# Performance work log

Measured on AMD Instinct MI355X. Metric: run time of the kernel, lower is better.

The kernel has to match this reference:

```python
import jax, jax.numpy as jnp
import numpy as np

VOCAB, EMB, HID, FC1, NCLS = 32000, 2048, 2048, 256, 3
T, B = 256, 128


def setup_inputs() -> dict:
    key = jax.random.key(0)
    ks = jax.random.split(key, 10)
    s_e = 1.0  # torch Embedding default init N(0,1)
    s_h = 1.0 / np.sqrt(HID)
    s_f1 = 1.0 / np.sqrt(HID)
    s_f2 = 1.0 / np.sqrt(FC1)
    return {
        "x": jax.random.randint(ks[0], (T, B), 0, VOCAB, dtype=jnp.int64)
        if jax.config.jax_enable_x64 else jax.random.randint(ks[0], (T, B), 0, VOCAB, dtype=jnp.int32),
        "emb": jax.random.normal(ks[1], (VOCAB, EMB), dtype=jnp.float32) * s_e,
        "W_ih": jax.random.uniform(ks[2], (HID, EMB), jnp.float32, -s_h, s_h),
        "W_hh": jax.random.uniform(ks[3], (HID, HID), jnp.float32, -s_h, s_h),
        "b_ih": jax.random.uniform(ks[4], (HID,), jnp.float32, -s_h, s_h),
        "b_hh": jax.random.uniform(ks[5], (HID,), jnp.float32, -s_h, s_h),
        "fc1_w": jax.random.uniform(ks[6], (FC1, HID), jnp.float32, -s_f1, s_f1),
        "fc1_b": jax.random.uniform(ks[7], (FC1,), jnp.float32, -s_f1, s_f1),
        "fc2_w": jax.random.uniform(ks[8], (NCLS, FC1), jnp.float32, -s_f2, s_f2),
        "fc2_b": jax.random.uniform(ks[9], (NCLS,), jnp.float32, -s_f2, s_f2),
    }


def reference(x, emb, W_ih, W_hh, b_ih, b_hh, fc1_w, fc1_b, fc2_w, fc2_b):
    # Embedding: [T, B] -> [T, B, E]
    xe = emb[x]
    # Precompute input projections for all steps in one big GEMM: [T, B, H]
    xproj = jnp.einsum("tbe,he->tbh", xe, W_ih) + b_ih + b_hh
    h0 = jnp.zeros((x.shape[1], W_hh.shape[0]), dtype=xe.dtype)

    def step(h, xp_t):
        h = jnp.tanh(xp_t + h @ W_hh.T)
        return h, None

    h_last, _ = jax.lax.scan(step, h0, xproj)
    # MLP head: hidden -> 256 -> relu -> 3
    z = jax.nn.relu(h_last @ fc1_w.T + fc1_b)
    return z @ fc2_w.T + fc2_b
```

## Files before the change

### kernel.cpp

```cpp
#include <hip/hip_runtime.h>

typedef _Float16 half8 __attribute__((ext_vector_type(8)));
typedef _Float16 half4v __attribute__((ext_vector_type(4)));
typedef float float4v __attribute__((ext_vector_type(4)));

#define HID 2048
#define EMBD 2048
#define BATCH 128
#define TSTEPS 256
#define STEP ((size_t)BATCH * HID)

__global__ __launch_bounds__(256) void cast_f16_kernel(const float* __restrict__ src,
                                                       _Float16* __restrict__ dst, int n) {
    int i = (blockIdx.x * 256 + threadIdx.x) * 4;
    int stride = gridDim.x * 256 * 4;
    for (; i < n; i += stride) {
        float4v v = *(const float4v*)(src + i);
        half4v h;
        h[0] = (_Float16)v[0]; h[1] = (_Float16)v[1];
        h[2] = (_Float16)v[2]; h[3] = (_Float16)v[3];
        *(half4v*)(dst + i) = h;
    }
}

__global__ __launch_bounds__(256) void bias_kernel(const float* __restrict__ a,
                                                   const float* __restrict__ b,
                                                   float* __restrict__ dst) {
    int i = blockIdx.x * 256 + threadIdx.x;
    if (i < HID) dst[i] = a[i] + b[i];
}

__global__ __launch_bounds__(256) void phaseA_kernel(const int* __restrict__ x,
                                                     const float* __restrict__ emb,
                                                     const _Float16* __restrict__ w16,
                                                     const float* __restrict__ bias,
                                                     _Float16* __restrict__ xproj) {
    __shared__ __align__(16) _Float16 As[128 * 64];
    __shared__ __align__(16) _Float16 Bs[128 * 64];

    const int tid = threadIdx.x;
    const int bx  = blockIdx.x;
    const int nt = bx & 15, mt = bx >> 4;
    const long m0 = (long)mt * 128;
    const long n0 = (long)nt * 128;
    const int lane = tid & 63, w = tid >> 6;
    const int ln15 = lane & 15, kg = lane >> 4;
    const int wr = (w >> 1) * 64, wc = (w & 1) * 64;

    int xr[4];
#pragma unroll
    for (int it = 0; it < 4; ++it) xr[it] = x[m0 + ((it * 256 + tid) >> 3)];

    float4v acc[4][4];
#pragma unroll
    for (int m = 0; m < 4; ++m)
#pragma unroll
        for (int n = 0; n < 4; ++n) acc[m][n] = (float4v){0.f, 0.f, 0.f, 0.f};

    for (int kt = 0; kt < 32; ++kt) {
        __syncthreads();
#pragma unroll
        for (int it = 0; it < 4; ++it) {
            int c = it * 256 + tid;
            const float* src = emb + (long)xr[it] * EMBD + kt * 64 + (c & 7) * 8;
            float4v v0 = *(const float4v*)src;
            float4v v1 = *(const float4v*)(src + 4);
            half8 hv;
#pragma unroll
            for (int q = 0; q < 4; ++q) { hv[q] = (_Float16)v0[q]; hv[4 + q] = (_Float16)v1[q]; }
            *(half8*)(&As[c * 8]) = hv;
        }
#pragma unroll
        for (int it = 0; it < 4; ++it) {
            int c = it * 256 + tid;
            const _Float16* src = w16 + (n0 + (c >> 3)) * (long)EMBD + kt * 64 + (c & 7) * 8;
            __builtin_amdgcn_global_load_lds((const __attribute__((address_space(1))) void*)src,
                                             (__attribute__((address_space(3))) void*)&Bs[c * 8],
                                             16, 0, 0);
        }
        __syncthreads();
#pragma unroll
        for (int kk = 0; kk < 2; ++kk) {
            half8 a[4], b[4];
#pragma unroll
            for (int m = 0; m < 4; ++m)
                a[m] = *(half8*)(&As[(wr + m * 16 + ln15) * 64 + kk * 32 + kg * 8]);
#pragma unroll
            for (int n = 0; n < 4; ++n)
                b[n] = *(half8*)(&Bs[(wc + n * 16 + ln15) * 64 + kk * 32 + kg * 8]);
#pragma unroll
            for (int m = 0; m < 4; ++m)
#pragma unroll
                for (int n = 0; n < 4; ++n)
                    acc[m][n] = __builtin_amdgcn_mfma_f32_16x16x32_f16(b[n], a[m], acc[m][n], 0, 0, 0);
        }
    }
#pragma unroll
    for (int m = 0; m < 4; ++m) {
        long mg = m0 + wr + m * 16 + ln15;
#pragma unroll
        for (int n = 0; n < 4; ++n) {
            int nb = (int)n0 + wc + n * 16 + kg * 4;
            float4v bv = *(const float4v*)(bias + nb);
            union { half4v h; unsigned long long u; } pk;
#pragma unroll
            for (int r = 0; r < 4; ++r) pk.h[r] = (_Float16)(acc[m][n][r] + bv[r]);
            *(unsigned long long*)(xproj + mg * HID + nb) = pk.u;
        }
    }
}

__global__ __launch_bounds__(256, 1) void scan_kernel(_Float16* __restrict__ xb,
                                                      const _Float16* __restrict__ whh,
                                                      float* __restrict__ hlast,
                                                      unsigned char* __restrict__ flags) {
    __shared__ __align__(16) _Float16 Wl[32 * 2048];
    __shared__ float part[4][16 * 33];

    const int tid = threadIdx.x;
    const int bx = blockIdx.x;
    const int gid = bx & 3, sub = bx >> 2;
    const int m0 = gid * 32, n0 = sub * 32;
    const int lane = tid & 63, w = tid >> 6;
    const int ln15 = lane & 15, kg = lane >> 4;
    const int pr = w >> 1, kh = w & 1;

    for (int it = 0; it < 32; ++it) {
        int c = it * 256 + tid;
        int col = c >> 8, ch = c & 255;
        half8 v = *(const half8*)(whh + (long)(n0 + col) * HID + ch * 8);
        *(half8*)((char*)Wl + col * 4096 + ((ch * 16) ^ ((col & 7) << 4))) = v;
    }
    __syncthreads();

    unsigned char* gfl = flags + gid * 64;
    const unsigned long long* gfl64 = (const unsigned long long*)gfl;
    const size_t arow = (size_t)(m0 + pr * 16 + ln15);
    const int wb0 = ln15 * 4096, wb1 = (16 + ln15) * 4096;
    const int swz = (ln15 & 7) << 4;
    const int kb = kh * 2048;
    const int rp = tid >> 7, ridx = tid & 127;
    const int rrow = ridx >> 3, rc4 = (ridx & 7) * 4;
    const size_t oidx = (size_t)(m0 + rp * 16 + rrow) * HID + n0 + rc4;

    for (int s = 0; s < TSTEPS; ++s) {
        unsigned long long xbits = __hip_atomic_load(
            (const unsigned long long*)(xb + (size_t)(s + 1) * STEP + oidx),
            __ATOMIC_RELAXED, __HIP_MEMORY_SCOPE_AGENT);

        float4v acc0 = (float4v){0.f, 0.f, 0.f, 0.f};
        float4v acc1 = (float4v){0.f, 0.f, 0.f, 0.f};
        if (s > 0) {
            unsigned long long pat =
                (unsigned long long)(unsigned char)(s - 1) * 0x0101010101010101ull;
            for (;;) {
                bool ok = true;
                if (lane < 8) {
                    unsigned long long v = __hip_atomic_load(gfl64 + lane,
                                            __ATOMIC_RELAXED, __HIP_MEMORY_SCOPE_AGENT);
                    unsigned long long xx = v ^ pat;
                    ok = !((xx - 0x0101010101010101ull) & ~xx & 0x8080808080808080ull);
                }
                if (__all(ok)) break;
            }
            asm volatile("" ::: "memory");
            __builtin_amdgcn_sched_barrier(0);

            const _Float16* hrow = xb + (size_t)(s - 1) * STEP + arow * HID + kh * 1024;
#pragma unroll
            for (int j = 0; j < 32; ++j) {
                half8 a = *(const half8*)(hrow + j * 32 + kg * 8);
                int k2 = kb + j * 64 + kg * 16;
                half8 b0 = *(half8*)((char*)Wl + wb0 + (k2 ^ swz));
                half8 b1 = *(half8*)((char*)Wl + wb1 + (k2 ^ swz));
                acc0 = __builtin_amdgcn_mfma_f32_16x16x32_f16(a, b0, acc0, 0, 0, 0);
                acc1 = __builtin_amdgcn_mfma_f32_16x16x32_f16(a, b1, acc1, 0, 0, 0);
            }
#pragma unroll
            for (int r = 0; r < 4; ++r) {
                part[w][(kg * 4 + r) * 33 + ln15] = acc0[r];
                part[w][(kg * 4 + r) * 33 + 16 + ln15] = acc1[r];
            }
        }

        float s0 = 0.f, s1 = 0.f, s2 = 0.f, s3 = 0.f;
        if (s > 0) {
            __syncthreads();
            const float* p0 = &part[2 * rp][rrow * 33 + rc4];
            const float* p1 = &part[2 * rp + 1][rrow * 33 + rc4];
            s0 = p0[0] + p1[0]; s1 = p0[1] + p1[1];
            s2 = p0[2] + p1[2]; s3 = p0[3] + p1[3];
        }
        union { unsigned long long u; half4v h; } xbv; xbv.u = xbits;
        float o0 = tanhf(s0 + (float)xbv.h[0]);
        float o1 = tanhf(s1 + (float)xbv.h[1]);
        float o2 = tanhf(s2 + (float)xbv.h[2]);
        float o3 = tanhf(s3 + (float)xbv.h[3]);

        if (s < TSTEPS - 1) {
            union { half4v h; unsigned long long u; } pk;
            pk.h[0] = (_Float16)o0; pk.h[1] = (_Float16)o1;
            pk.h[2] = (_Float16)o2; pk.h[3] = (_Float16)o3;
            __hip_atomic_store((unsigned long long*)(xb + (size_t)s * STEP + oidx),
                               pk.u, __ATOMIC_RELAXED, __HIP_MEMORY_SCOPE_AGENT);
            __syncthreads();
            if (tid == 0)
                __hip_atomic_store(&gfl[sub], (unsigned char)(s + 1),
                                   __ATOMIC_RELAXED, __HIP_MEMORY_SCOPE_AGENT);
        } else {
            float4v f = {o0, o1, o2, o3};
            *(float4v*)(hlast + oidx) = f;
        }
    }
}

__global__ __launch_bounds__(256) void fc1_kernel(const float* __restrict__ hlast,
                                                  const float* __restrict__ w,
                                                  const float* __restrict__ b,
                                                  float* __restrict__ z) {
    __shared__ float hs[8][256];
    const int blk = blockIdx.x;
    const int j = threadIdx.x;
    const int bb0 = blk * 8;
    float acc[8];
#pragma unroll
    for (int r = 0; r < 8; ++r) acc[r] = 0.f;
    const float* wr = w + (long)j * HID;
    const int sr = j >> 5, sc = (j & 31) * 8;

    for (int kt = 0; kt < 8; ++kt) {
        __syncthreads();
        float4v h0 = *(const float4v*)(hlast + (long)(bb0 + sr) * HID + kt * 256 + sc);
        float4v h1 = *(const float4v*)(hlast + (long)(bb0 + sr) * HID + kt * 256 + sc + 4);
        *(float4v*)&hs[sr][sc] = h0;
        *(float4v*)&hs[sr][sc + 4] = h1;
        __syncthreads();
        for (int k = 0; k < 256; k += 4) {
            float4v wv = *(const float4v*)(wr + kt * 256 + k);
#pragma unroll
            for (int r = 0; r < 8; ++r) {
                float4v hv = *(const float4v*)&hs[r][k];
                acc[r] += hv[0] * wv[0] + hv[1] * wv[1] + hv[2] * wv[2] + hv[3] * wv[3];
            }
        }
    }
    float bj = b[j];
#pragma unroll
    for (int r = 0; r < 8; ++r) z[(bb0 + r) * 256 + j] = fmaxf(acc[r] + bj, 0.f);
}

__global__ __launch_bounds__(256) void fc2_kernel(const float* __restrict__ z,
                                                  const float* __restrict__ w,
                                                  const float* __restrict__ b,
                                                  float* __restrict__ out) {
    __shared__ float red[4];
    int bb = blockIdx.x;
    int tid = threadIdx.x;
    float zv = z[bb * 256 + tid];
    for (int c = 0; c < 3; ++c) {
        float s = zv * w[c * 256 + tid];
        for (int off = 32; off > 0; off >>= 1) s += __shfl_down(s, off, 64);
        if ((tid & 63) == 0) red[tid >> 6] = s;
        __syncthreads();
        if (tid == 0) out[bb * 3 + c] = red[0] + red[1] + red[2] + red[3] + b[c];
        __syncthreads();
    }
}

extern "C" void kernel_launch(void* const* d_in, const int* in_sizes, int n_in,
                              void* d_out, int out_size, void* d_ws, size_t ws_size,
                              hipStream_t stream) {
    const int*   x    = (const int*)d_in[0];
    const float* emb  = (const float*)d_in[1];
    const float* Wih  = (const float*)d_in[2];
    const float* Whh  = (const float*)d_in[3];
    const float* bih  = (const float*)d_in[4];
    const float* bhh  = (const float*)d_in[5];
    const float* fc1w = (const float*)d_in[6];
    const float* fc1b = (const float*)d_in[7];
    const float* fc2w = (const float*)d_in[8];
    const float* fc2b = (const float*)d_in[9];
    float* out = (float*)d_out;

    char* ws = (char*)d_ws;
    size_t off = 0;
    _Float16* xb    = (_Float16*)(ws + off); off += 257 * STEP * 2;
    _Float16* wih16 = (_Float16*)(ws + off); off += (size_t)HID * EMBD * 2;
    _Float16* whh16 = (_Float16*)(ws + off); off += (size_t)HID * HID * 2;
    float*    bias  = (float*)(ws + off);    off += (size_t)HID * 4;
    float*    hlast = (float*)(ws + off);    off += (size_t)BATCH * HID * 4;
    float*    z     = (float*)(ws + off);    off += (size_t)BATCH * 256 * 4;
    unsigned char* flags = (unsigned char*)(ws + off); off += 256;

    hipMemsetAsync(flags, 0, 256, stream);

    cast_f16_kernel<<<4096, 256, 0, stream>>>(Wih, wih16, HID * EMBD);
    cast_f16_kernel<<<4096, 256, 0, stream>>>(Whh, whh16, HID * HID);
    bias_kernel<<<8, 256, 0, stream>>>(bih, bhh, bias);

    phaseA_kernel<<<4096, 256, 0, stream>>>(x, emb, wih16, bias, xb + STEP);

    void* args[] = {(void*)&xb, (void*)&whh16, (void*)&hlast, (void*)&flags};
    hipLaunchCooperativeKernel((const void*)scan_kernel, dim3(256), dim3(256), args, 0, stream);

    fc1_kernel<<<16, 256, 0, stream>>>(hlast, fc1w, fc1b, z);
    fc2_kernel<<<BATCH, 256, 0, stream>>>(z, fc2w, fc2b, out);
}
```

Baseline: 2.731 ms.

## Map scan blocks to XCDs with K-split pairs exchanging partial sums

Each scan block reads its hardware XCC id and takes a slot from a per-XCD atomic counter. Blocks are assigned so each XCD handles one batch group and one K half, with 64 output columns per block. Paired blocks on the two K halves exchange partial sums through a global buffer, and per-XCD flag arrays use monotonic counters plus s_sleep. The aim is to keep the h-state polling and traffic local to an XCD's L2 and to cut cross-XCD synchronization. The cost is an extra cross-block partial-sum handoff each step, and correctness relies on an even block distribution across XCDs. Phase A also replaces global_load_lds with a plain load and store.

```diff
diff --git a/kernel.cpp b/kernel.cpp
--- a/kernel.cpp
+++ b/kernel.cpp
@@ -74,9 +74,7 @@
         for (int it = 0; it < 4; ++it) {
             int c = it * 256 + tid;
             const _Float16* src = w16 + (n0 + (c >> 3)) * (long)EMBD + kt * 64 + (c & 7) * 8;
-            __builtin_amdgcn_global_load_lds((const __attribute__((address_space(1))) void*)src,
-                                             (__attribute__((address_space(3))) void*)&Bs[c * 8],
-                                             16, 0, 0);
+            *(half8*)(&Bs[c * 8]) = *(const half8*)src;
         }
         __syncthreads();
 #pragma unroll
@@ -113,103 +111,167 @@
 __global__ __launch_bounds__(256, 1) void scan_kernel(_Float16* __restrict__ xb,
                                                       const _Float16* __restrict__ whh,
                                                       float* __restrict__ hlast,
-                                                      unsigned char* __restrict__ flags) {
-    __shared__ __align__(16) _Float16 Wl[32 * 2048];
-    __shared__ float part[4][16 * 33];
+                                                      unsigned* __restrict__ ctrs,
+                                                      unsigned* __restrict__ pfl,
+                                                      unsigned* __restrict__ hfl,
+                                                      float* __restrict__ pexch) {
+    __shared__ __align__(16) _Float16 Wl[64 * 1024];
+    __shared__ __align__(16) float part[2][16 * 68];
+    __shared__ int sh_ids[2];
 
     const int tid = threadIdx.x;
-    const int bx = blockIdx.x;
-    const int gid = bx & 3, sub = bx >> 2;
-    const int m0 = gid * 32, n0 = sub * 32;
+    if (tid == 0) {
+        unsigned xcc;
+        asm volatile("s_getreg_b32 %0, hwreg(HW_REG_XCC_ID)" : "=s"(xcc));
+        unsigned slot = atomicAdd(&ctrs[xcc * 32], 1u);
+        sh_ids[0] = (int)xcc;
+        sh_ids[1] = (int)slot;
+    }
+    __syncthreads();
+    const int xcd = sh_ids[0], slot = sh_ids[1];
+    const int g = xcd >> 1, kh = xcd & 1, c = slot;
+    const int m0 = g * 32;
+    const long n0 = (long)c * 64;
+    const int kbase = kh * 1024;
+    const bool fin = (kh == 0) ? (c < 16) : (c >= 16);
+    const int pairid = g * 32 + c;
+    const int fi = (kh == 0) ? c : (c - 16);
+
+    for (int it = 0; it < 32; ++it) {
+        int idx = it * 256 + tid;
+        int col = idx >> 7, ch = idx & 127;
+        half8 v = *(const half8*)(whh + (n0 + col) * (long)HID + kbase + ch * 8);
+        *(half8*)((char*)Wl + col * 2048 + ((ch * 16) ^ ((col & 7) << 4))) = v;
+    }
+    __syncthreads();
+
     const int lane = tid & 63, w = tid >> 6;
     const int ln15 = lane & 15, kg = lane >> 4;
-    const int pr = w >> 1, kh = w & 1;
-
-    for (int it = 0; it < 32; ++it) {
-        int c = it * 256 + tid;
-        int col = c >> 8, ch = c & 255;
-        half8 v = *(const half8*)(whh + (long)(n0 + col) * HID + ch * 8);
-        *(half8*)((char*)Wl + col * 4096 + ((ch * 16) ^ ((col & 7) << 4))) = v;
-    }
-    __syncthreads();
-
-    unsigned char* gfl = flags + gid * 64;
-    const unsigned long long* gfl64 = (const unsigned long long*)gfl;
-    const size_t arow = (size_t)(m0 + pr * 16 + ln15);
-    const int wb0 = ln15 * 4096, wb1 = (16 + ln15) * 4096;
+    const int mi = w >> 1, kj = w & 1;
     const int swz = (ln15 & 7) << 4;
-    const int kb = kh * 2048;
-    const int rp = tid >> 7, ridx = tid & 127;
-    const int rrow = ridx >> 3, rc4 = (ridx & 7) * 4;
-    const size_t oidx = (size_t)(m0 + rp * 16 + rrow) * HID + n0 + rc4;
+    const size_t arow = (size_t)(m0 + mi * 16 + ln15);
+    const int prow = tid >> 3;
+    const int pc8 = (tid & 7) * 8;
+    const int pmi = prow >> 4;
+    const int ppo = (prow & 15) * 68 + pc8;
+    const size_t gidx = (size_t)(m0 + prow) * HID + n0 + pc8;
+    unsigned long long* pex64 = (unsigned long long*)pexch + (size_t)pairid * 1024
+                                + (size_t)(prow * 64 + pc8) / 2;
+    const unsigned long long* hfl64 = (const unsigned long long*)(hfl + xcd * 64);
 
     for (int s = 0; s < TSTEPS; ++s) {
-        unsigned long long xbits = __hip_atomic_load(
-            (const unsigned long long*)(xb + (size_t)(s + 1) * STEP + oidx),
-            __ATOMIC_RELAXED, __HIP_MEMORY_SCOPE_AGENT);
-
-        float4v acc0 = (float4v){0.f, 0.f, 0.f, 0.f};
-        float4v acc1 = (float4v){0.f, 0.f, 0.f, 0.f};
+        unsigned long long b0 = 0, b1 = 0;
+        if (fin) {
+            const unsigned long long* bp =
+                (const unsigned long long*)(xb + (size_t)(s + 1) * STEP + gidx);
+            b0 = __hip_atomic_load(bp, __ATOMIC_RELAXED, __HIP_MEMORY_SCOPE_AGENT);
+            b1 = __hip_atomic_load(bp + 1, __ATOMIC_RELAXED, __HIP_MEMORY_SCOPE_AGENT);
+        }
+
         if (s > 0) {
-            unsigned long long pat =
-                (unsigned long long)(unsigned char)(s - 1) * 0x0101010101010101ull;
             for (;;) {
                 bool ok = true;
                 if (lane < 8) {
-                    unsigned long long v = __hip_atomic_load(gfl64 + lane,
+                    unsigned long long v = __hip_atomic_load(hfl64 + lane,
                                             __ATOMIC_RELAXED, __HIP_MEMORY_SCOPE_AGENT);
-                    unsigned long long xx = v ^ pat;
-                    ok = !((xx - 0x0101010101010101ull) & ~xx & 0x8080808080808080ull);
+                    ok = ((unsigned)v >= (unsigned)s) && ((unsigned)(v >> 32) >= (unsigned)s);
                 }
                 if (__all(ok)) break;
+                __builtin_amdgcn_s_sleep(1);
             }
             asm volatile("" ::: "memory");
             __builtin_amdgcn_sched_barrier(0);
 
-            const _Float16* hrow = xb + (size_t)(s - 1) * STEP + arow * HID + kh * 1024;
-#pragma unroll
-            for (int j = 0; j < 32; ++j) {
+            const _Float16* hrow = xb + (size_t)(s - 1) * STEP + arow * HID + kbase + kj * 512;
+            float4v acc[4];
+#pragma unroll
+            for (int nf = 0; nf < 4; ++nf) acc[nf] = (float4v){0.f, 0.f, 0.f, 0.f};
+#pragma unroll
+            for (int j = 0; j < 16; ++j) {
                 half8 a = *(const half8*)(hrow + j * 32 + kg * 8);
-                int k2 = kb + j * 64 + kg * 16;
-                half8 b0 = *(half8*)((char*)Wl + wb0 + (k2 ^ swz));
-                half8 b1 = *(half8*)((char*)Wl + wb1 + (k2 ^ swz));
-                acc0 = __builtin_amdgcn_mfma_f32_16x16x32_f16(a, b0, acc0, 0, 0, 0);
-                acc1 = __builtin_amdgcn_mfma_f32_16x16x32_f16(a, b1, acc1, 0, 0, 0);
-            }
-#pragma unroll
-            for (int r = 0; r < 4; ++r) {
-                part[w][(kg * 4 + r) * 33 + ln15] = acc0[r];
-                part[w][(kg * 4 + r) * 33 + 16 + ln15] = acc1[r];
-            }
-        }
-
-        float s0 = 0.f, s1 = 0.f, s2 = 0.f, s3 = 0.f;
-        if (s > 0) {
+                int k2 = (kj * 512 + j * 32 + kg * 8) * 2;
+#pragma unroll
+                for (int nf = 0; nf < 4; ++nf) {
+                    half8 b = *(half8*)((char*)Wl + (nf * 16 + ln15) * 2048 + (k2 ^ swz));
+                    acc[nf] = __builtin_amdgcn_mfma_f32_16x16x32_f16(a, b, acc[nf], 0, 0, 0);
+                }
+            }
+            if (kj == 1) {
+#pragma unroll
+                for (int nf = 0; nf < 4; ++nf)
+#pragma unroll
+                    for (int r = 0; r < 4; ++r)
+                        part[mi][(kg * 4 + r) * 68 + nf * 16 + ln15] = acc[nf][r];
+            }
             __syncthreads();
-            const float* p0 = &part[2 * rp][rrow * 33 + rc4];
-            const float* p1 = &part[2 * rp + 1][rrow * 33 + rc4];
-            s0 = p0[0] + p1[0]; s1 = p0[1] + p1[1];
-            s2 = p0[2] + p1[2]; s3 = p0[3] + p1[3];
-        }
-        union { unsigned long long u; half4v h; } xbv; xbv.u = xbits;
-        float o0 = tanhf(s0 + (float)xbv.h[0]);
-        float o1 = tanhf(s1 + (float)xbv.h[1]);
-        float o2 = tanhf(s2 + (float)xbv.h[2]);
-        float o3 = tanhf(s3 + (float)xbv.h[3]);
-
-        if (s < TSTEPS - 1) {
-            union { half4v h; unsigned long long u; } pk;
-            pk.h[0] = (_Float16)o0; pk.h[1] = (_Float16)o1;
-            pk.h[2] = (_Float16)o2; pk.h[3] = (_Float16)o3;
-            __hip_atomic_store((unsigned long long*)(xb + (size_t)s * STEP + oidx),
-                               pk.u, __ATOMIC_RELAXED, __HIP_MEMORY_SCOPE_AGENT);
+            if (kj == 0) {
+#pragma unroll
+                for (int nf = 0; nf < 4; ++nf)
+#pragma unroll
+                    for (int r = 0; r < 4; ++r)
+                        part[mi][(kg * 4 + r) * 68 + nf * 16 + ln15] += acc[nf][r];
+            }
             __syncthreads();
-            if (tid == 0)
-                __hip_atomic_store(&gfl[sub], (unsigned char)(s + 1),
-                                   __ATOMIC_RELAXED, __HIP_MEMORY_SCOPE_AGENT);
+        }
+
+        if (!fin) {
+            if (s > 0) {
+                union { float4v f; unsigned long long u[2]; } ua, ub;
+                ua.f = *(const float4v*)&part[pmi][ppo];
+                ub.f = *(const float4v*)&part[pmi][ppo + 4];
+                __hip_atomic_store(pex64 + 0, ua.u[0], __ATOMIC_RELAXED, __HIP_MEMORY_SCOPE_AGENT);
+                __hip_atomic_store(pex64 + 1, ua.u[1], __ATOMIC_RELAXED, __HIP_MEMORY_SCOPE_AGENT);
+                __hip_atomic_store(pex64 + 2, ub.u[0], __ATOMIC_RELAXED, __HIP_MEMORY_SCOPE_AGENT);
+                __hip_atomic_store(pex64 + 3, ub.u[1], __ATOMIC_RELAXED, __HIP_MEMORY_SCOPE_AGENT);
+                __syncthreads();
+                if (tid == 0)
+                    __hip_atomic_store(&pfl[pairid], (unsigned)(s + 1),
+                                       __ATOMIC_RELAXED, __HIP_MEMORY_SCOPE_AGENT);
+            }
         } else {
-            float4v f = {o0, o1, o2, o3};
-            *(float4v*)(hlast + oidx) = f;
+            float o[8];
+            if (s > 0) {
+                while (__hip_atomic_load(&pfl[pairid], __ATOMIC_RELAXED,
+                                         __HIP_MEMORY_SCOPE_AGENT) <= (unsigned)s)
+                    __builtin_amdgcn_s_sleep(1);
+                asm volatile("" ::: "memory");
+                __builtin_amdgcn_sched_barrier(0);
+                union { unsigned long long u[2]; float f[4]; } va, vb;
+                va.u[0] = __hip_atomic_load(pex64 + 0, __ATOMIC_RELAXED, __HIP_MEMORY_SCOPE_AGENT);
+                va.u[1] = __hip_atomic_load(pex64 + 1, __ATOMIC_RELAXED, __HIP_MEMORY_SCOPE_AGENT);
+                vb.u[0] = __hip_atomic_load(pex64 + 2, __ATOMIC_RELAXED, __HIP_MEMORY_SCOPE_AGENT);
+                vb.u[1] = __hip_atomic_load(pex64 + 3, __ATOMIC_RELAXED, __HIP_MEMORY_SCOPE_AGENT);
+                float4v ma = *(const float4v*)&part[pmi][ppo];
+                float4v mb = *(const float4v*)&part[pmi][ppo + 4];
+#pragma unroll
+                for (int i = 0; i < 4; ++i) { o[i] = ma[i] + va.f[i]; o[4 + i] = mb[i] + vb.f[i]; }
+            } else {
+#pragma unroll
+                for (int i = 0; i < 8; ++i) o[i] = 0.f;
+            }
+            union { unsigned long long u; half4v h; } xv0, xv1;
+            xv0.u = b0; xv1.u = b1;
+            float t[8];
+#pragma unroll
+            for (int i = 0; i < 4; ++i) {
+                t[i]     = tanhf(o[i]     + (float)xv0.h[i]);
+                t[4 + i] = tanhf(o[4 + i] + (float)xv1.h[i]);
+            }
+            if (s < TSTEPS - 1) {
+                half8 hv;
+#pragma unroll
+                for (int i = 0; i < 8; ++i) hv[i] = (_Float16)t[i];
+                *(half8*)(xb + (size_t)s * STEP + gidx) = hv;
+                __syncthreads();
+                if (tid == 0)
+                    __hip_atomic_store(&hfl[xcd * 64 + fi], (unsigned)(s + 1),
+                                       __ATOMIC_RELAXED, __HIP_MEMORY_SCOPE_AGENT);
+            } else {
+                float4v f0 = {t[0], t[1], t[2], t[3]};
+                float4v f1 = {t[4], t[5], t[6], t[7]};
+                *(float4v*)(hlast + gidx) = f0;
+                *(float4v*)(hlast + gidx + 4) = f1;
+            }
         }
     }
 }
@@ -290,9 +352,12 @@
     float*    bias  = (float*)(ws + off);    off += (size_t)HID * 4;
     float*    hlast = (float*)(ws + off);    off += (size_t)BATCH * HID * 4;
     float*    z     = (float*)(ws + off);    off += (size_t)BATCH * 256 * 4;
-    unsigned char* flags = (unsigned char*)(ws + off); off += 256;
-
-    hipMemsetAsync(flags, 0, 256, stream);
+    unsigned* ctrs  = (unsigned*)(ws + off); off += 8 * 32 * 4;
+    unsigned* pfl   = (unsigned*)(ws + off); off += 128 * 4;
+    unsigned* hfl   = (unsigned*)(ws + off); off += 8 * 64 * 4;
+    float*    pexch = (float*)(ws + off);    off += (size_t)128 * 2048 * 4;
+
+    hipMemsetAsync(ctrs, 0, (8 * 32 + 128 + 8 * 64) * 4, stream);
 
     cast_f16_kernel<<<4096, 256, 0, stream>>>(Wih, wih16, HID * EMBD);
     cast_f16_kernel<<<4096, 256, 0, stream>>>(Whh, whh16, HID * HID);
@@ -300,7 +365,8 @@
 
     phaseA_kernel<<<4096, 256, 0, stream>>>(x, emb, wih16, bias, xb + STEP);
 
-    void* args[] = {(void*)&xb, (void*)&whh16, (void*)&hlast, (void*)&flags};
+    void* args[] = {(void*)&xb, (void*)&whh16, (void*)&hlast,
+                    (void*)&ctrs, (void*)&pfl, (void*)&hfl, (void*)&pexch};
     hipLaunchCooperativeKernel((const void*)scan_kernel, dim3(256), dim3(256), args, 0, stream);
 
     fc1_kernel<<<16, 256, 0, stream>>>(hlast, fc1w, fc1b, z);
```

Result: slower. 3.171 ms (+16.1%).

## Fuse input-projection GEMM into persistent scan kernel with lookahead

Applied to the files above, without the earlier changes.

Removes the separate phaseA GEMM and bias kernels and has each scan workgroup compute its own slice of the input projection (embedding gather times W_ih plus both biases) a few timesteps ahead, inside the latency-bound recurrence loop. The aim is to hide the large projection GEMM behind the idle time the scan spends spinning on cross-block flags. Flags become 32-bit step counters compared with >=, and the spin loop sleeps between polls. The cost is that each workgroup streams W_ih rows and embedding rows from global memory with no LDS reuse, which can lengthen each step of the critical path.

```diff
diff --git a/kernel.cpp b/kernel.cpp
--- a/kernel.cpp
+++ b/kernel.cpp
@@ -9,6 +9,7 @@
 #define BATCH 128
 #define TSTEPS 256
 #define STEP ((size_t)BATCH * HID)
+#define LOOK 4
 
 __global__ __launch_bounds__(256) void cast_f16_kernel(const float* __restrict__ src,
                                                        _Float16* __restrict__ dst, int n) {
@@ -23,97 +24,15 @@
     }
 }
 
-__global__ __launch_bounds__(256) void bias_kernel(const float* __restrict__ a,
-                                                   const float* __restrict__ b,
-                                                   float* __restrict__ dst) {
-    int i = blockIdx.x * 256 + threadIdx.x;
-    if (i < HID) dst[i] = a[i] + b[i];
-}
-
-__global__ __launch_bounds__(256) void phaseA_kernel(const int* __restrict__ x,
-                                                     const float* __restrict__ emb,
-                                                     const _Float16* __restrict__ w16,
-                                                     const float* __restrict__ bias,
-                                                     _Float16* __restrict__ xproj) {
-    __shared__ __align__(16) _Float16 As[128 * 64];
-    __shared__ __align__(16) _Float16 Bs[128 * 64];
-
-    const int tid = threadIdx.x;
-    const int bx  = blockIdx.x;
-    const int nt = bx & 15, mt = bx >> 4;
-    const long m0 = (long)mt * 128;
-    const long n0 = (long)nt * 128;
-    const int lane = tid & 63, w = tid >> 6;
-    const int ln15 = lane & 15, kg = lane >> 4;
-    const int wr = (w >> 1) * 64, wc = (w & 1) * 64;
-
-    int xr[4];
-#pragma unroll
-    for (int it = 0; it < 4; ++it) xr[it] = x[m0 + ((it * 256 + tid) >> 3)];
-
-    float4v acc[4][4];
-#pragma unroll
-    for (int m = 0; m < 4; ++m)
-#pragma unroll
-        for (int n = 0; n < 4; ++n) acc[m][n] = (float4v){0.f, 0.f, 0.f, 0.f};
-
-    for (int kt = 0; kt < 32; ++kt) {
-        __syncthreads();
-#pragma unroll
-        for (int it = 0; it < 4; ++it) {
-            int c = it * 256 + tid;
-            const float* src = emb + (long)xr[it] * EMBD + kt * 64 + (c & 7) * 8;
-            float4v v0 = *(const float4v*)src;
-            float4v v1 = *(const float4v*)(src + 4);
-            half8 hv;
-#pragma unroll
-            for (int q = 0; q < 4; ++q) { hv[q] = (_Float16)v0[q]; hv[4 + q] = (_Float16)v1[q]; }
-            *(half8*)(&As[c * 8]) = hv;
-        }
-#pragma unroll
-        for (int it = 0; it < 4; ++it) {
-            int c = it * 256 + tid;
-            const _Float16* src = w16 + (n0 + (c >> 3)) * (long)EMBD + kt * 64 + (c & 7) * 8;
-            __builtin_amdgcn_global_load_lds((const __attribute__((address_space(1))) void*)src,
-                                             (__attribute__((address_space(3))) void*)&Bs[c * 8],
-                                             16, 0, 0);
-        }
-        __syncthreads();
-#pragma unroll
-        for (int kk = 0; kk < 2; ++kk) {
-            half8 a[4], b[4];
-#pragma unroll
-            for (int m = 0; m < 4; ++m)
-                a[m] = *(half8*)(&As[(wr + m * 16 + ln15) * 64 + kk * 32 + kg * 8]);
-#pragma unroll
-            for (int n = 0; n < 4; ++n)
-                b[n] = *(half8*)(&Bs[(wc + n * 16 + ln15) * 64 + kk * 32 + kg * 8]);
-#pragma unroll
-            for (int m = 0; m < 4; ++m)
-#pragma unroll
-                for (int n = 0; n < 4; ++n)
-                    acc[m][n] = __builtin_amdgcn_mfma_f32_16x16x32_f16(b[n], a[m], acc[m][n], 0, 0, 0);
-        }
-    }
-#pragma unroll
-    for (int m = 0; m < 4; ++m) {
-        long mg = m0 + wr + m * 16 + ln15;
-#pragma unroll
-        for (int n = 0; n < 4; ++n) {
-            int nb = (int)n0 + wc + n * 16 + kg * 4;
-            float4v bv = *(const float4v*)(bias + nb);
-            union { half4v h; unsigned long long u; } pk;
-#pragma unroll
-            for (int r = 0; r < 4; ++r) pk.h[r] = (_Float16)(acc[m][n][r] + bv[r]);
-            *(unsigned long long*)(xproj + mg * HID + nb) = pk.u;
-        }
-    }
-}
-
 __global__ __launch_bounds__(256, 1) void scan_kernel(_Float16* __restrict__ xb,
                                                       const _Float16* __restrict__ whh,
+                                                      const _Float16* __restrict__ wih,
+                                                      const float* __restrict__ emb,
+                                                      const int* __restrict__ xtok,
+                                                      const float* __restrict__ bih,
+                                                      const float* __restrict__ bhh,
                                                       float* __restrict__ hlast,
-                                                      unsigned char* __restrict__ flags) {
+                                                      unsigned* __restrict__ flags) {
     __shared__ __align__(16) _Float16 Wl[32 * 2048];
     __shared__ float part[4][16 * 33];
 
@@ -133,7 +52,7 @@
     }
     __syncthreads();
 
-    unsigned char* gfl = flags + gid * 64;
+    unsigned* gfl = flags + gid * 64;
     const unsigned long long* gfl64 = (const unsigned long long*)gfl;
     const size_t arow = (size_t)(m0 + pr * 16 + ln15);
     const int wb0 = ln15 * 4096, wb1 = (16 + ln15) * 4096;
@@ -143,6 +62,40 @@
     const int rrow = ridx >> 3, rc4 = (ridx & 7) * 4;
     const size_t oidx = (size_t)(m0 + rp * 16 + rrow) * HID + n0 + rc4;
 
+    const int trowg = m0 + pr * 16 + ln15;
+    const int tcol = n0 + kh * 16 + kg * 4;
+    const _Float16* bwrow = wih + (size_t)(n0 + kh * 16 + ln15) * EMBD;
+    float4v breg = *(const float4v*)(bih + tcol);
+    { float4v b2 = *(const float4v*)(bhh + tcol); breg = breg + b2; }
+
+    auto tileA = [&](int t) {
+        int tok = xtok[t * BATCH + trowg];
+        const float* ae = emb + (size_t)tok * EMBD;
+        float4v ta0 = (float4v){0.f, 0.f, 0.f, 0.f};
+        float4v ta1 = (float4v){0.f, 0.f, 0.f, 0.f};
+#pragma unroll 16
+        for (int j = 0; j < 64; ++j) {
+            int k = j * 32 + kg * 8;
+            float4v e0 = *(const float4v*)(ae + k);
+            float4v e1 = *(const float4v*)(ae + k + 4);
+            half8 a;
+#pragma unroll
+            for (int q = 0; q < 4; ++q) { a[q] = (_Float16)e0[q]; a[4 + q] = (_Float16)e1[q]; }
+            half8 bw = *(const half8*)(bwrow + k);
+            if (j & 1) ta1 = __builtin_amdgcn_mfma_f32_16x16x32_f16(bw, a, ta1, 0, 0, 0);
+            else       ta0 = __builtin_amdgcn_mfma_f32_16x16x32_f16(bw, a, ta0, 0, 0, 0);
+        }
+        union { half4v h; unsigned long long u; } pk;
+#pragma unroll
+        for (int r = 0; r < 4; ++r) pk.h[r] = (_Float16)(ta0[r] + ta1[r] + breg[r]);
+        __hip_atomic_store((unsigned long long*)(xb + (size_t)(t + 1) * STEP +
+                                                 (size_t)trowg * HID + tcol),
+                           pk.u, __ATOMIC_RELAXED, __HIP_MEMORY_SCOPE_AGENT);
+    };
+
+    for (int t = 0; t < LOOK; ++t) tileA(t);
+    asm volatile("s_waitcnt vmcnt(0)" ::: "memory");
+
     for (int s = 0; s < TSTEPS; ++s) {
         unsigned long long xbits = __hip_atomic_load(
             (const unsigned long long*)(xb + (size_t)(s + 1) * STEP + oidx),
@@ -151,17 +104,15 @@
         float4v acc0 = (float4v){0.f, 0.f, 0.f, 0.f};
         float4v acc1 = (float4v){0.f, 0.f, 0.f, 0.f};
         if (s > 0) {
-            unsigned long long pat =
-                (unsigned long long)(unsigned char)(s - 1) * 0x0101010101010101ull;
             for (;;) {
                 bool ok = true;
-                if (lane < 8) {
+                if (lane < 32) {
                     unsigned long long v = __hip_atomic_load(gfl64 + lane,
                                             __ATOMIC_RELAXED, __HIP_MEMORY_SCOPE_AGENT);
-                    unsigned long long xx = v ^ pat;
-                    ok = !((xx - 0x0101010101010101ull) & ~xx & 0x8080808080808080ull);
+                    ok = ((unsigned)v >= (unsigned)s) && ((unsigned)(v >> 32) >= (unsigned)s);
                 }
                 if (__all(ok)) break;
+                __builtin_amdgcn_s_sleep(2);
             }
             asm volatile("" ::: "memory");
             __builtin_amdgcn_sched_barrier(0);
@@ -205,12 +156,14 @@
                                pk.u, __ATOMIC_RELAXED, __HIP_MEMORY_SCOPE_AGENT);
             __syncthreads();
             if (tid == 0)
-                __hip_atomic_store(&gfl[sub], (unsigned char)(s + 1),
+                __hip_atomic_store(&gfl[sub], (unsigned)(s + 1),
                                    __ATOMIC_RELAXED, __HIP_MEMORY_SCOPE_AGENT);
         } else {
             float4v f = {o0, o1, o2, o3};
             *(float4v*)(hlast + oidx) = f;
         }
+
+        if (s + LOOK < TSTEPS) tileA(s + LOOK);
     }
 }
 
@@ -287,20 +240,17 @@
     _Float16* xb    = (_Float16*)(ws + off); off += 257 * STEP * 2;
     _Float16* wih16 = (_Float16*)(ws + off); off += (size_t)HID * EMBD * 2;
     _Float16* whh16 = (_Float16*)(ws + off); off += (size_t)HID * HID * 2;
-    float*    bias  = (float*)(ws + off);    off += (size_t)HID * 4;
     float*    hlast = (float*)(ws + off);    off += (size_t)BATCH * HID * 4;
     float*    z     = (float*)(ws + off);    off += (size_t)BATCH * 256 * 4;
-    unsigned char* flags = (unsigned char*)(ws + off); off += 256;
-
-    hipMemsetAsync(flags, 0, 256, stream);
+    unsigned* flags = (unsigned*)(ws + off); off += 4 * 64 * 4;
+
+    hipMemsetAsync(flags, 0, 4 * 64 * 4, stream);
 
     cast_f16_kernel<<<4096, 256, 0, stream>>>(Wih, wih16, HID * EMBD);
     cast_f16_kernel<<<4096, 256, 0, stream>>>(Whh, whh16, HID * HID);
-    bias_kernel<<<8, 256, 0, stream>>>(bih, bhh, bias);
-
-    phaseA_kernel<<<4096, 256, 0, stream>>>(x, emb, wih16, bias, xb + STEP);
-
-    void* args[] = {(void*)&xb, (void*)&whh16, (void*)&hlast, (void*)&flags};
+
+    void* args[] = {(void*)&xb, (void*)&whh16, (void*)&wih16, (void*)&emb,
+                    (void*)&x, (void*)&bih, (void*)&bhh, (void*)&hlast, (void*)&flags};
     hipLaunchCooperativeKernel((const void*)scan_kernel, dim3(256), dim3(256), args, 0, stream);
 
     fc1_kernel<<<16, 256, 0, stream>>>(hlast, fc1w, fc1b, z);
```

New measurement: 9.716 ms. +255.8%, slower.

## Partition RNN scan by XCD with register-resident weights and per-wave flags

Applied to the files above, without the earlier changes.

Reworks the persistent scan kernel so each block reads its hardware XCC id and takes a slot from a per-XCD atomic counter. Each XCD then owns 16 batch rows, and that group's dependency flags stay within one die. Each wave now computes a full 16x16 output tile over the whole K dimension, with half of W_hh in LDS and half held in registers. This removes the LDS partial-sum reduction and the block-wide syncs per step, replaced by per-wave flag stores and polling with s_sleep. It also swaps global_load_lds for a plain load/store in phase A, and relies on the hardware scheduler giving exactly 32 blocks per XCD, which brings large register pressure and a correctness risk.

```diff
diff --git a/kernel.cpp b/kernel.cpp
--- a/kernel.cpp
+++ b/kernel.cpp
@@ -74,9 +74,7 @@
         for (int it = 0; it < 4; ++it) {
             int c = it * 256 + tid;
             const _Float16* src = w16 + (n0 + (c >> 3)) * (long)EMBD + kt * 64 + (c & 7) * 8;
-            __builtin_amdgcn_global_load_lds((const __attribute__((address_space(1))) void*)src,
-                                             (__attribute__((address_space(3))) void*)&Bs[c * 8],
-                                             16, 0, 0);
+            *(half8*)(&Bs[c * 8]) = *(const half8*)src;
         }
         __syncthreads();
 #pragma unroll
@@ -113,35 +111,49 @@
 __global__ __launch_bounds__(256, 1) void scan_kernel(_Float16* __restrict__ xb,
                                                       const _Float16* __restrict__ whh,
                                                       float* __restrict__ hlast,
-                                                      unsigned char* __restrict__ flags) {
-    __shared__ __align__(16) _Float16 Wl[32 * 2048];
-    __shared__ float part[4][16 * 33];
+                                                      unsigned* __restrict__ ctrs,
+                                                      unsigned* __restrict__ flags) {
+    __shared__ __align__(16) _Float16 Wl[64 * 1024];
+    __shared__ int sh_ids[2];
 
     const int tid = threadIdx.x;
-    const int bx = blockIdx.x;
-    const int gid = bx & 3, sub = bx >> 2;
-    const int m0 = gid * 32, n0 = sub * 32;
+    if (tid == 0) {
+        unsigned xcc;
+        asm volatile("s_getreg_b32 %0, hwreg(HW_REG_XCC_ID)" : "=s"(xcc));
+        sh_ids[0] = (int)xcc;
+        sh_ids[1] = (int)atomicAdd(&ctrs[xcc * 32], 1u);
+    }
+    __syncthreads();
+    const int xcd = sh_ids[0], c = sh_ids[1];
+    const int m0 = xcd * 16;
+    const long n0 = (long)c * 64;
+
+    for (int it = 0; it < 32; ++it) {
+        int idx = it * 256 + tid;
+        int col = idx >> 7, ch = idx & 127;
+        half8 v = *(const half8*)(whh + (n0 + col) * (long)HID + ch * 8);
+        *(half8*)((char*)Wl + col * 2048 + ((ch * 16) ^ ((col & 7) << 4))) = v;
+    }
+
     const int lane = tid & 63, w = tid >> 6;
     const int ln15 = lane & 15, kg = lane >> 4;
-    const int pr = w >> 1, kh = w & 1;
-
-    for (int it = 0; it < 32; ++it) {
-        int c = it * 256 + tid;
-        int col = c >> 8, ch = c & 255;
-        half8 v = *(const half8*)(whh + (long)(n0 + col) * HID + ch * 8);
-        *(half8*)((char*)Wl + col * 4096 + ((ch * 16) ^ ((col & 7) << 4))) = v;
+    const int swz = (ln15 & 7) << 4;
+    const int wbyte = (16 * w + ln15) * 2048;
+
+    half8 wreg[32];
+    {
+        const _Float16* wsrc = whh + (n0 + 16 * w + ln15) * (long)HID + 1024 + kg * 8;
+#pragma unroll
+        for (int j = 0; j < 32; ++j) wreg[j] = *(const half8*)(wsrc + j * 32);
     }
     __syncthreads();
 
-    unsigned char* gfl = flags + gid * 64;
+    unsigned* gfl = flags + xcd * 128;
     const unsigned long long* gfl64 = (const unsigned long long*)gfl;
-    const size_t arow = (size_t)(m0 + pr * 16 + ln15);
-    const int wb0 = ln15 * 4096, wb1 = (16 + ln15) * 4096;
-    const int swz = (ln15 & 7) << 4;
-    const int kb = kh * 2048;
-    const int rp = tid >> 7, ridx = tid & 127;
-    const int rrow = ridx >> 3, rc4 = (ridx & 7) * 4;
-    const size_t oidx = (size_t)(m0 + rp * 16 + rrow) * HID + n0 + rc4;
+    const size_t hrowoff = (size_t)(m0 + ln15) * HID;
+    const int ocol = (int)n0 + 16 * w + kg * 4;
+    const size_t oidx = hrowoff + ocol;
+    const int fidx = c * 4 + w;
 
     for (int s = 0; s < TSTEPS; ++s) {
         unsigned long long xbits = __hip_atomic_load(
@@ -151,61 +163,46 @@
         float4v acc0 = (float4v){0.f, 0.f, 0.f, 0.f};
         float4v acc1 = (float4v){0.f, 0.f, 0.f, 0.f};
         if (s > 0) {
-            unsigned long long pat =
-                (unsigned long long)(unsigned char)(s - 1) * 0x0101010101010101ull;
             for (;;) {
-                bool ok = true;
-                if (lane < 8) {
-                    unsigned long long v = __hip_atomic_load(gfl64 + lane,
-                                            __ATOMIC_RELAXED, __HIP_MEMORY_SCOPE_AGENT);
-                    unsigned long long xx = v ^ pat;
-                    ok = !((xx - 0x0101010101010101ull) & ~xx & 0x8080808080808080ull);
-                }
+                unsigned long long v = __hip_atomic_load(gfl64 + lane,
+                                        __ATOMIC_RELAXED, __HIP_MEMORY_SCOPE_AGENT);
+                bool ok = ((unsigned)v >= (unsigned)s) && ((unsigned)(v >> 32) >= (unsigned)s);
                 if (__all(ok)) break;
+                __builtin_amdgcn_s_sleep(2);
             }
             asm volatile("" ::: "memory");
             __builtin_amdgcn_sched_barrier(0);
 
-            const _Float16* hrow = xb + (size_t)(s - 1) * STEP + arow * HID + kh * 1024;
+            const _Float16* hrow = xb + (size_t)(s - 1) * STEP + hrowoff + kg * 8;
 #pragma unroll
             for (int j = 0; j < 32; ++j) {
-                half8 a = *(const half8*)(hrow + j * 32 + kg * 8);
-                int k2 = kb + j * 64 + kg * 16;
-                half8 b0 = *(half8*)((char*)Wl + wb0 + (k2 ^ swz));
-                half8 b1 = *(half8*)((char*)Wl + wb1 + (k2 ^ swz));
-                acc0 = __builtin_amdgcn_mfma_f32_16x16x32_f16(a, b0, acc0, 0, 0, 0);
-                acc1 = __builtin_amdgcn_mfma_f32_16x16x32_f16(a, b1, acc1, 0, 0, 0);
+                half8 a = *(const half8*)(hrow + j * 32);
+                half8 b = *(half8*)((char*)Wl + wbyte + ((j * 64 + kg * 16) ^ swz));
+                if (j & 1) acc1 = __builtin_amdgcn_mfma_f32_16x16x32_f16(b, a, acc1, 0, 0, 0);
+                else       acc0 = __builtin_amdgcn_mfma_f32_16x16x32_f16(b, a, acc0, 0, 0, 0);
             }
 #pragma unroll
-            for (int r = 0; r < 4; ++r) {
-                part[w][(kg * 4 + r) * 33 + ln15] = acc0[r];
-                part[w][(kg * 4 + r) * 33 + 16 + ln15] = acc1[r];
+            for (int j = 0; j < 32; ++j) {
+                half8 a = *(const half8*)(hrow + 1024 + j * 32);
+                if (j & 1) acc1 = __builtin_amdgcn_mfma_f32_16x16x32_f16(wreg[j], a, acc1, 0, 0, 0);
+                else       acc0 = __builtin_amdgcn_mfma_f32_16x16x32_f16(wreg[j], a, acc0, 0, 0, 0);
             }
         }
 
-        float s0 = 0.f, s1 = 0.f, s2 = 0.f, s3 = 0.f;
-        if (s > 0) {
-            __syncthreads();
-            const float* p0 = &part[2 * rp][rrow * 33 + rc4];
-            const float* p1 = &part[2 * rp + 1][rrow * 33 + rc4];
-            s0 = p0[0] + p1[0]; s1 = p0[1] + p1[1];
-            s2 = p0[2] + p1[2]; s3 = p0[3] + p1[3];
-        }
         union { unsigned long long u; half4v h; } xbv; xbv.u = xbits;
-        float o0 = tanhf(s0 + (float)xbv.h[0]);
-        float o1 = tanhf(s1 + (float)xbv.h[1]);
-        float o2 = tanhf(s2 + (float)xbv.h[2]);
-        float o3 = tanhf(s3 + (float)xbv.h[3]);
+        float o0 = tanhf(acc0[0] + acc1[0] + (float)xbv.h[0]);
+        float o1 = tanhf(acc0[1] + acc1[1] + (float)xbv.h[1]);
+        float o2 = tanhf(acc0[2] + acc1[2] + (float)xbv.h[2]);
+        float o3 = tanhf(acc0[3] + acc1[3] + (float)xbv.h[3]);
 
         if (s < TSTEPS - 1) {
             union { half4v h; unsigned long long u; } pk;
             pk.h[0] = (_Float16)o0; pk.h[1] = (_Float16)o1;
             pk.h[2] = (_Float16)o2; pk.h[3] = (_Float16)o3;
-            __hip_atomic_store((unsigned long long*)(xb + (size_t)s * STEP + oidx),
-                               pk.u, __ATOMIC_RELAXED, __HIP_MEMORY_SCOPE_AGENT);
-            __syncthreads();
-            if (tid == 0)
-                __hip_atomic_store(&gfl[sub], (unsigned char)(s + 1),
+            *(unsigned long long*)(xb + (size_t)s * STEP + oidx) = pk.u;
+            asm volatile("s_waitcnt vmcnt(0)" ::: "memory");
+            if (lane == 0)
+                __hip_atomic_store(&gfl[fidx], (unsigned)(s + 1),
                                    __ATOMIC_RELAXED, __HIP_MEMORY_SCOPE_AGENT);
         } else {
             float4v f = {o0, o1, o2, o3};
@@ -290,9 +287,10 @@
     float*    bias  = (float*)(ws + off);    off += (size_t)HID * 4;
     float*    hlast = (float*)(ws + off);    off += (size_t)BATCH * HID * 4;
     float*    z     = (float*)(ws + off);    off += (size_t)BATCH * 256 * 4;
-    unsigned char* flags = (unsigned char*)(ws + off); off += 256;
-
-    hipMemsetAsync(flags, 0, 256, stream);
+    unsigned* ctrs  = (unsigned*)(ws + off); off += 8 * 32 * 4;
+    unsigned* flags = (unsigned*)(ws + off); off += 8 * 128 * 4;
+
+    hipMemsetAsync(ctrs, 0, (8 * 32 + 8 * 128) * 4, stream);
 
     cast_f16_kernel<<<4096, 256, 0, stream>>>(Wih, wih16, HID * EMBD);
     cast_f16_kernel<<<4096, 256, 0, stream>>>(Whh, whh16, HID * HID);
@@ -300,7 +298,7 @@
 
     phaseA_kernel<<<4096, 256, 0, stream>>>(x, emb, wih16, bias, xb + STEP);
 
-    void* args[] = {(void*)&xb, (void*)&whh16, (void*)&hlast, (void*)&flags};
+    void* args[] = {(void*)&xb, (void*)&whh16, (void*)&hlast, (void*)&ctrs, (void*)&flags};
     hipLaunchCooperativeKernel((const void*)scan_kernel, dim3(256), dim3(256), args, 0, stream);
 
     fc1_kernel<<<16, 256, 0, stream>>>(hlast, fc1w, fc1b, z);
```

After: 4.355 ms. +59.4%, slower.
